# Kernel tuning notes

Measured on AMD Instinct MI355X. Metric: run time of the kernel, lower is better.

The kernel has to match this reference:

```python
import jax, jax.numpy as jnp
import numpy as np

B, S, H, D = 4, 2048, 12, 64
WINDOW = 128          # local_attention window => (w//2, w//2) sliding window
BASE = 16000.0        # rope theta (ProkBert default)
NEG = -1e9


def rotate_half(x):
    x1, x2 = jnp.split(x, 2, axis=-1)
    return jnp.concatenate([-x2, x1], axis=-1)


def setup_inputs() -> dict:
    key = jax.random.key(0)
    k1, = jax.random.split(key, 1)
    qkv = jax.random.normal(k1, (B, S, 3, H, D), dtype=jnp.float32)
    pos = jnp.arange(S)
    inv_freq = 1.0 / (BASE ** (jnp.arange(0, D, 2).astype(jnp.float32) / D))
    freqs = pos[:, None].astype(jnp.float32) * inv_freq[None, :]   # (S, D/2)
    emb = jnp.concatenate([freqs, freqs], axis=-1)                  # (S, D)
    cos = jnp.cos(emb)
    sin = jnp.sin(emb)
    dist = jnp.abs(pos[:, None] - pos[None, :])
    mask = jnp.where(dist <= WINDOW // 2, 0.0, NEG).astype(jnp.float32)[None, None]  # (1,1,S,S)
    return {"qkv": qkv, "cos": cos, "sin": sin, "mask": mask}


def reference(qkv, cos, sin, mask):
    # qkv: (B, S, 3, H, D) -> q/k/v: (B, H, S, D)
    q = jnp.swapaxes(qkv[:, :, 0], 1, 2)
    k = jnp.swapaxes(qkv[:, :, 1], 1, 2)
    v = jnp.swapaxes(qkv[:, :, 2], 1, 2)
    cos_b = cos[None, None]   # (1,1,S,D)
    sin_b = sin[None, None]
    q = q * cos_b + rotate_half(q) * sin_b
    k = k * cos_b + rotate_half(k) * sin_b
    scale = D ** -0.5
    scores = jnp.einsum('bhqd,bhkd->bhqk', q, k) * scale + mask
    w = jax.nn.softmax(scores.astype(jnp.float32), axis=-1).astype(q.dtype)
    out = jnp.einsum('bhqk,bhkd->bhqd', w, v)
    out = jnp.swapaxes(out, 1, 2).reshape(B, S, H * D)  # (B, S, dim)
    return out
```

## Files before the change

### kernel.cpp

```cpp
#include <hip/hip_runtime.h>
#include <hip/hip_bf16.h>
#include <cstdint>


typedef short bf16x8 __attribute__((ext_vector_type(8)));
typedef float f32x4  __attribute__((ext_vector_type(4)));
typedef uint32_t u32x4 __attribute__((ext_vector_type(4)));

#define SLEN   2048
#define NHEAD  12
#define NBATCH 4
#define HD     64
#define WHALF  64
#define QT     64
#define KROWS  192
#define NKC    9
#define VST    68
#define VROWS  96
#define QSCALE 0.18033688011112042f


__device__ __forceinline__ uint32_t cvt_pk(float lo, float hi) {
    uint32_t r;
    asm("v_cvt_pk_bf16_f32 %0, %1, %2" : "=v"(r) : "v"(lo), "v"(hi));
    return r;
}

__global__ __launch_bounds__(256, 6) void prokbert_attn(
        const float* __restrict__ qkv, const float* __restrict__ cosT,
        const float* __restrict__ sinT, float* __restrict__ out)
{
    __shared__ __align__(16) uint32_t sbuf[VROWS * VST];
    short* sKp = (short*)sbuf;

    const int tid = threadIdx.x;

    const int bid = blockIdx.x;
    const int gid = (bid & 7) * 192 + (bid >> 3);
    const int qt = gid & 31;
    const int hh = gid >> 5;
    const int h = hh % NHEAD, b = hh / NHEAD;

    const int q0 = qt * QT;
    const int kstart = q0 - WHALF;

    const int wv = tid >> 6;
    const int lane = tid & 63;
    const int r = lane & 15, g = lane >> 4;
    const int rx = r & 7;
    const int qrow = q0 + wv * 16 + r;

    const int rrb = tid >> 2, c4 = tid & 3, d0 = c4 * 8;

#define LOADK(IT, S) \
    f32x4 xl0##S, xl1##S, xh0##S, xh1##S, cc0##S, cc1##S, ss0##S, ss1##S; \
    { \
        const int s = kstart + rrb + (IT) * 64; \
        if ((unsigned)s < SLEN) { \
            const size_t kbase = (((size_t)(b * SLEN + s) * 3 + 1) * NHEAD + h) * HD; \
            const f32x4* gxl = (const f32x4*)(qkv + kbase + d0); \
            const f32x4* gxh = (const f32x4*)(qkv + kbase + d0 + 32); \
            const f32x4* gc  = (const f32x4*)(cosT + s * HD + d0); \
            const f32x4* gs  = (const f32x4*)(sinT + s * HD + d0); \
            xl0##S = gxl[0]; xl1##S = gxl[1]; \
            xh0##S = gxh[0]; xh1##S = gxh[1]; \
            cc0##S = gc[0];  cc1##S = gc[1]; \
            ss0##S = gs[0];  ss1##S = gs[1]; \
        } else { \
            const f32x4 z = {0.f, 0.f, 0.f, 0.f}; \
            xl0##S = z; xl1##S = z; xh0##S = z; xh1##S = z; \
            cc0##S = z; cc1##S = z; ss0##S = z; ss1##S = z; \
        } \
    }

#define CONVSTOREK(IT, S) \
    { \
        const int rr = rrb + (IT) * 64; \
        u32x4 klo, khi; \
         \
        klo[0] = cvt_pk(xl0##S[0] * cc0##S[0] - xh0##S[0] * ss0##S[0], \
                        xl0##S[1] * cc0##S[1] - xh0##S[1] * ss0##S[1]); \
        klo[1] = cvt_pk(xl0##S[2] * cc0##S[2] - xh0##S[2] * ss0##S[2], \
                        xl0##S[3] * cc0##S[3] - xh0##S[3] * ss0##S[3]); \
        klo[2] = cvt_pk(xl1##S[0] * cc1##S[0] - xh1##S[0] * ss1##S[0], \
                        xl1##S[1] * cc1##S[1] - xh1##S[1] * ss1##S[1]); \
        klo[3] = cvt_pk(xl1##S[2] * cc1##S[2] - xh1##S[2] * ss1##S[2], \
                        xl1##S[3] * cc1##S[3] - xh1##S[3] * ss1##S[3]); \
        khi[0] = cvt_pk(xh0##S[0] * cc0##S[0] + xl0##S[0] * ss0##S[0], \
                        xh0##S[1] * cc0##S[1] + xl0##S[1] * ss0##S[1]); \
        khi[1] = cvt_pk(xh0##S[2] * cc0##S[2] + xl0##S[2] * ss0##S[2], \
                        xh0##S[3] * cc0##S[3] + xl0##S[3] * ss0##S[3]); \
        khi[2] = cvt_pk(xh1##S[0] * cc1##S[0] + xl1##S[0] * ss1##S[0], \
                        xh1##S[1] * cc1##S[1] + xl1##S[1] * ss1##S[1]); \
        khi[3] = cvt_pk(xh1##S[2] * cc1##S[2] + xl1##S[2] * ss1##S[2], \
                        xh1##S[3] * cc1##S[3] + xl1##S[3] * ss1##S[3]); \
        const int sw = rr & 7; \
        *(u32x4*)&sKp[rr * 64 + ((c4 ^ sw) << 3)]       = klo; \
        *(u32x4*)&sKp[rr * 64 + (((c4 + 4) ^ sw) << 3)] = khi; \
    }

    {
        LOADK(0, a)
        LOADK(1, bb)
        CONVSTOREK(0, a)
        LOADK(2, cc)
        CONVSTOREK(1, bb)
        CONVSTOREK(2, cc)
    }
#undef LOADK
#undef CONVSTOREK

    bf16x8 qf0, qf1;
    {
        const size_t qb = (((size_t)(b * SLEN + qrow) * 3 + 0) * NHEAD + h) * HD;
        const f32x4* ga  = (const f32x4*)(qkv + qb + g * 8);
        const f32x4* gb  = (const f32x4*)(qkv + qb + 32 + g * 8);
        const f32x4* gc0 = (const f32x4*)(cosT + (size_t)qrow * HD + g * 8);
        const f32x4* gs0 = (const f32x4*)(sinT + (size_t)qrow * HD + g * 8);
        f32x4 qa0 = ga[0], qa1 = ga[1], qb0 = gb[0], qb1 = gb[1];
        f32x4 qc0 = gc0[0], qc1 = gc0[1], qs0 = gs0[0], qs1 = gs0[1];
        u32x4 w0, w1;
        w0[0] = cvt_pk((qa0[0] * qc0[0] - qb0[0] * qs0[0]) * QSCALE,
                       (qa0[1] * qc0[1] - qb0[1] * qs0[1]) * QSCALE);
        w0[1] = cvt_pk((qa0[2] * qc0[2] - qb0[2] * qs0[2]) * QSCALE,
                       (qa0[3] * qc0[3] - qb0[3] * qs0[3]) * QSCALE);
        w0[2] = cvt_pk((qa1[0] * qc1[0] - qb1[0] * qs1[0]) * QSCALE,
                       (qa1[1] * qc1[1] - qb1[1] * qs1[1]) * QSCALE);
        w0[3] = cvt_pk((qa1[2] * qc1[2] - qb1[2] * qs1[2]) * QSCALE,
                       (qa1[3] * qc1[3] - qb1[3] * qs1[3]) * QSCALE);
        w1[0] = cvt_pk((qb0[0] * qc0[0] + qa0[0] * qs0[0]) * QSCALE,
                       (qb0[1] * qc0[1] + qa0[1] * qs0[1]) * QSCALE);
        w1[1] = cvt_pk((qb0[2] * qc0[2] + qa0[2] * qs0[2]) * QSCALE,
                       (qb0[3] * qc0[3] + qa0[3] * qs0[3]) * QSCALE);
        w1[2] = cvt_pk((qb1[0] * qc1[0] + qa1[0] * qs1[0]) * QSCALE,
                       (qb1[1] * qc1[1] + qa1[1] * qs1[1]) * QSCALE);
        w1[3] = cvt_pk((qb1[2] * qc1[2] + qa1[2] * qs1[2]) * QSCALE,
                       (qb1[3] * qc1[3] + qa1[3] * qs1[3]) * QSCALE);
        qf0 = __builtin_bit_cast(bf16x8, w0);
        qf1 = __builtin_bit_cast(bf16x8, w1);
    }
    __syncthreads();

    f32x4 sc[NKC];
    #pragma unroll
    for (int kc = 0; kc < NKC; ++kc) {
        const int row = wv * 16 + kc * 16 + r;
        const bf16x8 ka0 = *(const bf16x8*)&sKp[row * 64 + ((g ^ rx) << 3)];
        const bf16x8 ka1 = *(const bf16x8*)&sKp[row * 64 + (((g + 4) ^ rx) << 3)];
        f32x4 c = {0.f, 0.f, 0.f, 0.f};
        c = __builtin_amdgcn_mfma_f32_16x16x32_bf16(ka0, qf0, c, 0, 0, 0);
        c = __builtin_amdgcn_mfma_f32_16x16x32_bf16(ka1, qf1, c, 0, 0, 0);
        sc[kc] = c;
    }

    const int tg = 4 * g;
    float sum = 0.f;
    #pragma unroll
    for (int kc = 0; kc < NKC; ++kc) {
        #pragma unroll
        for (int i = 0; i < 4; ++i) {
            float e = exp2f(sc[kc][i]);
            if (kc == 0) e = (tg + i >= r) ? e : 0.f;
            if (kc == 8) e = (tg + i <= r) ? e : 0.f;
            sc[kc][i] = e;
            sum += e;
        }
    }
    sum += __shfl_xor(sum, 16);
    sum += __shfl_xor(sum, 32);
    const int oob = max(0, WHALF - qrow) + max(0, qrow - (SLEN - 1 - WHALF));
    const float inv = 1.f / (sum - (float)oob);

    u32x4 paw[5];
    #pragma unroll
    for (int kb = 0; kb < 4; ++kb) {
        paw[kb][0] = cvt_pk(sc[2 * kb][0], sc[2 * kb][1]);
        paw[kb][1] = cvt_pk(sc[2 * kb][2], sc[2 * kb][3]);
        paw[kb][2] = cvt_pk(sc[2 * kb + 1][0], sc[2 * kb + 1][1]);
        paw[kb][3] = cvt_pk(sc[2 * kb + 1][2], sc[2 * kb + 1][3]);
    }
    paw[4][0] = cvt_pk(sc[8][0], sc[8][1]);
    paw[4][1] = cvt_pk(sc[8][2], sc[8][3]);
    paw[4][2] = 0; paw[4][3] = 0;

    f32x4 va[3][2], vb[3][2];
    #pragma unroll
    for (int it = 0; it < 3; ++it) {
        const int j = tid + it * 256;
        const int kp = j >> 3, dd = (j & 7) * 8;
        const int s0 = kstart + 2 * kp, s1 = s0 + 1;
        const f32x4 z = {0.f, 0.f, 0.f, 0.f};
        if ((unsigned)s0 < SLEN) {
            const f32x4* g0 = (const f32x4*)(qkv +
                (((size_t)(b * SLEN + s0) * 3 + 2) * NHEAD + h) * HD + dd);
            va[it][0] = g0[0]; va[it][1] = g0[1];
        } else { va[it][0] = z; va[it][1] = z; }
        if ((unsigned)s1 < SLEN) {
            const f32x4* g1 = (const f32x4*)(qkv +
                (((size_t)(b * SLEN + s1) * 3 + 2) * NHEAD + h) * HD + dd);
            vb[it][0] = g1[0]; vb[it][1] = g1[1];
        } else { vb[it][0] = z; vb[it][1] = z; }
    }
    __syncthreads();

    #pragma unroll
    for (int it = 0; it < 3; ++it) {
        const int j = tid + it * 256;
        const int kp = j >> 3, dd = (j & 7) * 8;
        u32x4 w0, w1;
        w0[0] = cvt_pk(va[it][0][0], vb[it][0][0]);
        w0[1] = cvt_pk(va[it][0][1], vb[it][0][1]);
        w0[2] = cvt_pk(va[it][0][2], vb[it][0][2]);
        w0[3] = cvt_pk(va[it][0][3], vb[it][0][3]);
        w1[0] = cvt_pk(va[it][1][0], vb[it][1][0]);
        w1[1] = cvt_pk(va[it][1][1], vb[it][1][1]);
        w1[2] = cvt_pk(va[it][1][2], vb[it][1][2]);
        w1[3] = cvt_pk(va[it][1][3], vb[it][1][3]);
        *(u32x4*)&sbuf[kp * VST + dd]     = w0;
        *(u32x4*)&sbuf[kp * VST + dd + 4] = w1;
    }
    __syncthreads();

    const uint32_t* vptr = &sbuf[(wv * 8 + 2 * g) * VST + r];
    f32x4 oacc[4] = {{0,0,0,0},{0,0,0,0},{0,0,0,0},{0,0,0,0}};
    #pragma unroll
    for (int kb = 0; kb < 5; ++kb) {
        const bf16x8 pa = __builtin_bit_cast(bf16x8, paw[kb]);
        #pragma unroll
        for (int dc = 0; dc < 4; ++dc) {
            const int base = kb * 16 * VST + dc * 16;
            u32x4 w;
            w[0] = vptr[base];
            w[1] = vptr[base + VST];
            if (kb < 4) {
                w[2] = vptr[base + 8 * VST];
                w[3] = vptr[base + 9 * VST];
            } else {
                w[2] = 0; w[3] = 0;
            }
            const bf16x8 vbf = __builtin_bit_cast(bf16x8, w);
            oacc[dc] = __builtin_amdgcn_mfma_f32_16x16x32_bf16(pa, vbf, oacc[dc], 0, 0, 0);
        }
    }

    #pragma unroll
    for (int i = 0; i < 4; ++i) {
        const float iq = __shfl(inv, g * 4 + i);
        const int qg = q0 + wv * 16 + g * 4 + i;
        float* orow = out + (((size_t)(b * SLEN + qg)) * NHEAD + h) * HD + r;
        orow[0]  = oacc[0][i] * iq;
        orow[16] = oacc[1][i] * iq;
        orow[32] = oacc[2][i] * iq;
        orow[48] = oacc[3][i] * iq;
    }
}

extern "C" void kernel_launch(void* const* d_in, const int* in_sizes, int n_in,
                              void* d_out, int out_size, void* d_ws, size_t ws_size,
                              hipStream_t stream) {
    const float* qkv  = (const float*)d_in[0];
    const float* cosT = (const float*)d_in[1];
    const float* sinT = (const float*)d_in[2];
    float* out = (float*)d_out;
    dim3 grid(32 * NHEAD * NBATCH);
    dim3 block(256);
    hipLaunchKernelGGL(prokbert_attn, grid, block, 0, stream, qkv, cosT, sinT, out);
}
```

Before: 31.13 us.

## Issue V loads upfront with separate K/V shared buffers and fused QK-softmax

Gives K and V their own shared-memory buffers so V no longer reuses K's space. The V global loads now issue at kernel start, overlapping their latency with the K/Q RoPE work, and one barrier is dropped. The QK MFMA, exp and bf16 packing are merged into one loop. In exchange, holding V in registers across the K phase and the larger shared footprint raise register and LDS pressure, and launch bounds drop from 6 to 3, which may lower occupancy.

```diff
diff --git a/kernel.cpp b/kernel.cpp
--- a/kernel.cpp
+++ b/kernel.cpp
@@ -26,12 +26,12 @@
     return r;
 }
 
-__global__ __launch_bounds__(256, 6) void prokbert_attn(
+__global__ __launch_bounds__(256, 3) void prokbert_attn(
         const float* __restrict__ qkv, const float* __restrict__ cosT,
         const float* __restrict__ sinT, float* __restrict__ out)
 {
-    __shared__ __align__(16) uint32_t sbuf[VROWS * VST];
-    short* sKp = (short*)sbuf;
+    __shared__ __align__(16) short    sK[KROWS * 64];
+    __shared__ __align__(16) uint32_t sV[VROWS * VST];
 
     const int tid = threadIdx.x;
 
@@ -49,6 +49,25 @@
     const int r = lane & 15, g = lane >> 4;
     const int rx = r & 7;
     const int qrow = q0 + wv * 16 + r;
+
+    f32x4 va[3][2], vb[3][2];
+    #pragma unroll
+    for (int it = 0; it < 3; ++it) {
+        const int j = tid + it * 256;
+        const int kp = j >> 3, dd = (j & 7) * 8;
+        const int s0 = kstart + 2 * kp, s1 = s0 + 1;
+        const f32x4 z = {0.f, 0.f, 0.f, 0.f};
+        if ((unsigned)s0 < SLEN) {
+            const f32x4* g0 = (const f32x4*)(qkv +
+                (((size_t)(b * SLEN + s0) * 3 + 2) * NHEAD + h) * HD + dd);
+            va[it][0] = g0[0]; va[it][1] = g0[1];
+        } else { va[it][0] = z; va[it][1] = z; }
+        if ((unsigned)s1 < SLEN) {
+            const f32x4* g1 = (const f32x4*)(qkv +
+                (((size_t)(b * SLEN + s1) * 3 + 2) * NHEAD + h) * HD + dd);
+            vb[it][0] = g1[0]; vb[it][1] = g1[1];
+        } else { vb[it][0] = z; vb[it][1] = z; }
+    }
 
     const int rrb = tid >> 2, c4 = tid & 3, d0 = c4 * 8;
 
@@ -95,8 +114,8 @@
         khi[3] = cvt_pk(xh1##S[2] * cc1##S[2] + xl1##S[2] * ss1##S[2], \
                         xh1##S[3] * cc1##S[3] + xl1##S[3] * ss1##S[3]); \
         const int sw = rr & 7; \
-        *(u32x4*)&sKp[rr * 64 + ((c4 ^ sw) << 3)]       = klo; \
-        *(u32x4*)&sKp[rr * 64 + (((c4 + 4) ^ sw) << 3)] = khi; \
+        *(u32x4*)&sK[rr * 64 + ((c4 ^ sw) << 3)]       = klo; \
+        *(u32x4*)&sK[rr * 64 + (((c4 + 4) ^ sw) << 3)] = khi; \
     }
 
     {
@@ -139,69 +158,6 @@
         qf0 = __builtin_bit_cast(bf16x8, w0);
         qf1 = __builtin_bit_cast(bf16x8, w1);
     }
-    __syncthreads();
-
-    f32x4 sc[NKC];
-    #pragma unroll
-    for (int kc = 0; kc < NKC; ++kc) {
-        const int row = wv * 16 + kc * 16 + r;
-        const bf16x8 ka0 = *(const bf16x8*)&sKp[row * 64 + ((g ^ rx) << 3)];
-        const bf16x8 ka1 = *(const bf16x8*)&sKp[row * 64 + (((g + 4) ^ rx) << 3)];
-        f32x4 c = {0.f, 0.f, 0.f, 0.f};
-        c = __builtin_amdgcn_mfma_f32_16x16x32_bf16(ka0, qf0, c, 0, 0, 0);
-        c = __builtin_amdgcn_mfma_f32_16x16x32_bf16(ka1, qf1, c, 0, 0, 0);
-        sc[kc] = c;
-    }
-
-    const int tg = 4 * g;
-    float sum = 0.f;
-    #pragma unroll
-    for (int kc = 0; kc < NKC; ++kc) {
-        #pragma unroll
-        for (int i = 0; i < 4; ++i) {
-            float e = exp2f(sc[kc][i]);
-            if (kc == 0) e = (tg + i >= r) ? e : 0.f;
-            if (kc == 8) e = (tg + i <= r) ? e : 0.f;
-            sc[kc][i] = e;
-            sum += e;
-        }
-    }
-    sum += __shfl_xor(sum, 16);
-    sum += __shfl_xor(sum, 32);
-    const int oob = max(0, WHALF - qrow) + max(0, qrow - (SLEN - 1 - WHALF));
-    const float inv = 1.f / (sum - (float)oob);
-
-    u32x4 paw[5];
-    #pragma unroll
-    for (int kb = 0; kb < 4; ++kb) {
-        paw[kb][0] = cvt_pk(sc[2 * kb][0], sc[2 * kb][1]);
-        paw[kb][1] = cvt_pk(sc[2 * kb][2], sc[2 * kb][3]);
-        paw[kb][2] = cvt_pk(sc[2 * kb + 1][0], sc[2 * kb + 1][1]);
-        paw[kb][3] = cvt_pk(sc[2 * kb + 1][2], sc[2 * kb + 1][3]);
-    }
-    paw[4][0] = cvt_pk(sc[8][0], sc[8][1]);
-    paw[4][1] = cvt_pk(sc[8][2], sc[8][3]);
-    paw[4][2] = 0; paw[4][3] = 0;
-
-    f32x4 va[3][2], vb[3][2];
-    #pragma unroll
-    for (int it = 0; it < 3; ++it) {
-        const int j = tid + it * 256;
-        const int kp = j >> 3, dd = (j & 7) * 8;
-        const int s0 = kstart + 2 * kp, s1 = s0 + 1;
-        const f32x4 z = {0.f, 0.f, 0.f, 0.f};
-        if ((unsigned)s0 < SLEN) {
-            const f32x4* g0 = (const f32x4*)(qkv +
-                (((size_t)(b * SLEN + s0) * 3 + 2) * NHEAD + h) * HD + dd);
-            va[it][0] = g0[0]; va[it][1] = g0[1];
-        } else { va[it][0] = z; va[it][1] = z; }
-        if ((unsigned)s1 < SLEN) {
-            const f32x4* g1 = (const f32x4*)(qkv +
-                (((size_t)(b * SLEN + s1) * 3 + 2) * NHEAD + h) * HD + dd);
-            vb[it][0] = g1[0]; vb[it][1] = g1[1];
-        } else { vb[it][0] = z; vb[it][1] = z; }
-    }
-    __syncthreads();
 
     #pragma unroll
     for (int it = 0; it < 3; ++it) {
@@ -216,12 +172,45 @@
         w1[1] = cvt_pk(va[it][1][1], vb[it][1][1]);
         w1[2] = cvt_pk(va[it][1][2], vb[it][1][2]);
         w1[3] = cvt_pk(va[it][1][3], vb[it][1][3]);
-        *(u32x4*)&sbuf[kp * VST + dd]     = w0;
-        *(u32x4*)&sbuf[kp * VST + dd + 4] = w1;
-    }
+        *(u32x4*)&sV[kp * VST + dd]     = w0;
+        *(u32x4*)&sV[kp * VST + dd + 4] = w1;
+    }
+
     __syncthreads();
 
-    const uint32_t* vptr = &sbuf[(wv * 8 + 2 * g) * VST + r];
+    u32x4 paw[5];
+    float sum = 0.f;
+    const int tg = 4 * g;
+    #pragma unroll
+    for (int kc = 0; kc < NKC; ++kc) {
+        const int row = wv * 16 + kc * 16 + r;
+        const bf16x8 ka0 = *(const bf16x8*)&sK[row * 64 + ((g ^ rx) << 3)];
+        const bf16x8 ka1 = *(const bf16x8*)&sK[row * 64 + (((g + 4) ^ rx) << 3)];
+        f32x4 c = {0.f, 0.f, 0.f, 0.f};
+        c = __builtin_amdgcn_mfma_f32_16x16x32_bf16(ka0, qf0, c, 0, 0, 0);
+        c = __builtin_amdgcn_mfma_f32_16x16x32_bf16(ka1, qf1, c, 0, 0, 0);
+        f32x4 e;
+        #pragma unroll
+        for (int i = 0; i < 4; ++i) {
+            float ev = exp2f(c[i]);
+            if (kc == 0) ev = (tg + i >= r) ? ev : 0.f;
+            if (kc == 8) ev = (tg + i <= r) ? ev : 0.f;
+            e[i] = ev;
+            sum += ev;
+        }
+        const uint32_t wlo = cvt_pk(e[0], e[1]);
+        const uint32_t whi = cvt_pk(e[2], e[3]);
+        if ((kc & 1) == 0) { paw[kc >> 1][0] = wlo; paw[kc >> 1][1] = whi; }
+        else               { paw[kc >> 1][2] = wlo; paw[kc >> 1][3] = whi; }
+    }
+    paw[4][2] = 0; paw[4][3] = 0;
+
+    sum += __shfl_xor(sum, 16);
+    sum += __shfl_xor(sum, 32);
+    const int oob = max(0, WHALF - qrow) + max(0, qrow - (SLEN - 1 - WHALF));
+    const float inv = 1.f / (sum - (float)oob);
+
+    const uint32_t* vptr = &sV[(wv * 8 + 2 * g) * VST + r];
     f32x4 oacc[4] = {{0,0,0,0},{0,0,0,0},{0,0,0,0},{0,0,0,0}};
     #pragma unroll
     for (int kb = 0; kb < 5; ++kb) {
```

Result: faster. 27.95 us (-10.2%).
